# Kernel optimization log

Hardware: AMD Instinct MI355X
Metric: run time of the kernel (lower is better)

## Reference

```python
import jax, jax.numpy as jnp
import numpy as np

N_PEP = 50000
N_PROT = 50000
H = 256
F_IN = 1280
E = 300000
EL = 200000


def setup_inputs() -> dict:
    key = jax.random.key(0)
    ks = jax.random.split(key, 16)
    s = 0.02
    return {
        "x_pep": jax.random.normal(ks[0], (N_PEP, F_IN), jnp.float32),
        "x_prot": jax.random.normal(ks[1], (N_PROT, F_IN), jnp.float32),
        "Wpep": s * jax.random.normal(ks[2], (H, F_IN), jnp.float32),
        "bpep": jnp.zeros((H,), jnp.float32),
        "Wprot": s * jax.random.normal(ks[3], (H, F_IN), jnp.float32),
        "bprot": jnp.zeros((H,), jnp.float32),
        "Wl1": s * jax.random.normal(ks[4], (3, H, H), jnp.float32),
        "bl1": jnp.zeros((3, H), jnp.float32),
        "Wr1": s * jax.random.normal(ks[5], (3, H, H), jnp.float32),
        "Wl2": s * jax.random.normal(ks[6], (3, H, H), jnp.float32),
        "bl2": jnp.zeros((3, H), jnp.float32),
        "Wr2": s * jax.random.normal(ks[7], (3, H, H), jnp.float32),
        "ei_pp": jax.random.randint(ks[8], (2, E), 0, N_PEP, jnp.int32),   # pep -> prot
        "ei_rp": jax.random.randint(ks[9], (2, E), 0, N_PROT, jnp.int32),  # prot -> pep (reverse)
        "ei_prot": jax.random.randint(ks[10], (2, E), 0, N_PROT, jnp.int32),  # prot -> prot
        "eli_het": jax.random.randint(ks[11], (2, EL), 0, N_PEP, jnp.int32),
        "eli_homo": jax.random.randint(ks[12], (2, EL), 0, N_PROT, jnp.int32),
    }


def _seg_mean(src_feat, dst_idx, n_dst):
    # mean aggregation of edge messages into destination nodes
    s = jax.ops.segment_sum(src_feat, dst_idx, num_segments=n_dst)
    cnt = jax.ops.segment_sum(jnp.ones((dst_idx.shape[0], 1), src_feat.dtype), dst_idx, num_segments=n_dst)
    return s / jnp.maximum(cnt, 1.0)


def _sage(x_src, x_dst, ei, Wl, bl, Wr):
    # PyG SAGEConv(aggr='mean'): lin_l(mean_j x_j) + lin_r(x_i); lin_r has no bias
    m = _seg_mean(x_src[ei[0]], ei[1], x_dst.shape[0])
    return m @ Wl.T + bl + x_dst @ Wr.T


def reference(x_pep, x_prot, Wpep, bpep, Wprot, bprot,
              Wl1, bl1, Wr1, Wl2, bl2, Wr2,
              ei_pp, ei_rp, ei_prot, eli_het, eli_homo):
    # feat_src == 'esm': linear projection of ESM features
    h_pep = x_pep @ Wpep.T + bpep
    h_prot = x_prot @ Wprot.T + bprot

    # --- hetero SAGE layer 1 (to_hetero: sum over edge types per dst type) ---
    p1 = jax.nn.relu(_sage(h_prot, h_pep, ei_rp, Wl1[1], bl1[1], Wr1[1]))
    q1 = jax.nn.relu(_sage(h_pep, h_prot, ei_pp, Wl1[0], bl1[0], Wr1[0])
                     + _sage(h_prot, h_prot, ei_prot, Wl1[2], bl1[2], Wr1[2]))

    # --- hetero SAGE layer 2 ---
    p2 = _sage(q1, p1, ei_rp, Wl2[1], bl2[1], Wr2[1])
    q2 = (_sage(p1, q1, ei_pp, Wl2[0], bl2[0], Wr2[0])
          + _sage(q1, q1, ei_prot, Wl2[2], bl2[2], Wr2[2]))

    # edge classifiers: gather + elementwise mul + sum
    het_pred = (p2[eli_het[0]] * q2[eli_het[1]]).sum(axis=-1)
    homo_pred = (q2[eli_homo[0]] * q2[eli_homo[1]]).sum(axis=-1)
    return (het_pred, homo_pred)
```

## Files before the change

### kernel.cpp

```cpp
#include <hip/hip_runtime.h>

using u16 = unsigned short;
using u32 = unsigned int;

#define H 256
#define NNODE 50000
#define CAP 32
#define BM 128
#define BN 128
#define BK 64

typedef __attribute__((ext_vector_type(8))) short bf16x8;
typedef __attribute__((ext_vector_type(4))) float f32x4;

struct AChunks { const void* p[5]; };

__device__ __forceinline__ u16 f2b(float f) {
    u32 u = __builtin_bit_cast(u32, f);
    return (u16)((u + 0x7FFFu + ((u >> 16) & 1u)) >> 16);
}
__device__ __forceinline__ float b2f(u16 h) {
    u32 u = ((u32)h) << 16;
    return __builtin_bit_cast(float, u);
}
__device__ __forceinline__ void gld_lds16(const void* g, void* l) {
    __builtin_amdgcn_global_load_lds(
        (__attribute__((address_space(1))) void*)(void*)g,
        (__attribute__((address_space(3))) void*)l, 16, 0, 0);
}
__device__ __forceinline__ u32 packbf(float a, float b) {
    return (u32)f2b(a) | ((u32)f2b(b) << 16);
}

template<bool RELU>
__global__ __launch_bounds__(512) void gemm_pipe(
    AChunks ac, int aStride, const u16* __restrict__ Bw,
    const float* __restrict__ bias, u16* __restrict__ C, int M, int Ktot)
{
    __shared__ __align__(16) char As[2][BM * 128];
    __shared__ __align__(16) char Bs[2][BN * 128];

    const int tid = threadIdx.x;
    const int l   = tid & 63;
    const int w   = tid >> 6;
    const int wr  = w >> 2, wc = w & 3;
    const int m0  = blockIdx.x * BM;
    const int n0  = blockIdx.y * BN;
    const int nk  = Ktot >> 6;

    f32x4 acc[4][2];
#pragma unroll
    for (int i = 0; i < 4; ++i)
#pragma unroll
        for (int j = 0; j < 2; ++j) acc[i][j] = f32x4{0.f, 0.f, 0.f, 0.f};

    auto stageB = [&](int k, int bi) {
        int k0 = k * 64;
#pragma unroll
        for (int i = 0; i < 2; ++i) {
            int ci = i * 512 + tid;
            int r = ci >> 3, c16 = ci & 7;
            int sb = (c16 * 16) ^ ((r & 7) << 4);
            const u16* g = Bw + (size_t)(n0 + r) * Ktot + k0 + (sb >> 1);
            gld_lds16(g, &Bs[bi][ci * 16]);
        }
    };
    auto stageAb = [&](int k, int bi) {
        int k0 = k * 64;
        const u16* base = (const u16*)ac.p[k0 >> 8];
        int kk = k0 & 255;
#pragma unroll
        for (int i = 0; i < 2; ++i) {
            int ci = i * 512 + tid;
            int r = ci >> 3, c16 = ci & 7;
            int row = m0 + r; row = row < M ? row : M - 1;
            int sb = (c16 * 16) ^ ((r & 7) << 4);
            const u16* g = base + (size_t)row * aStride + kk + (sb >> 1);
            gld_lds16(g, &As[bi][ci * 16]);
        }
    };
    auto compute = [&](int bi) {
#pragma unroll
        for (int ks = 0; ks < 2; ++ks) {
            bf16x8 af[4], bfr[2];
#pragma unroll
            for (int mi = 0; mi < 4; ++mi) {
                int r = wr * 64 + mi * 16 + (l & 15);
                int off = (ks * 64 + (l >> 4) * 16) ^ ((r & 7) << 4);
                af[mi] = *(const bf16x8*)&As[bi][r * 128 + off];
            }
#pragma unroll
            for (int ni = 0; ni < 2; ++ni) {
                int r = wc * 32 + ni * 16 + (l & 15);
                int off = (ks * 64 + (l >> 4) * 16) ^ ((r & 7) << 4);
                bfr[ni] = *(const bf16x8*)&Bs[bi][r * 128 + off];
            }
#pragma unroll
            for (int mi = 0; mi < 4; ++mi)
#pragma unroll
                for (int ni = 0; ni < 2; ++ni)
                    acc[mi][ni] = __builtin_amdgcn_mfma_f32_16x16x32_bf16(
                        af[mi], bfr[ni], acc[mi][ni], 0, 0, 0);
        }
    };
    auto body = [&](int k, int cur) {
        asm volatile("s_waitcnt vmcnt(4)" ::: "memory");
        __builtin_amdgcn_sched_barrier(0);
        __builtin_amdgcn_s_barrier();
        __builtin_amdgcn_sched_barrier(0);
        compute(cur);
        __builtin_amdgcn_sched_barrier(0);
        __builtin_amdgcn_s_barrier();
        __builtin_amdgcn_sched_barrier(0);
        int kq = k + 2; if (kq > nk - 1) kq = nk - 1;
        stageB(kq, cur);
        stageAb(kq, cur);
        __builtin_amdgcn_sched_barrier(0);
    };

    stageB(0, 0); stageAb(0, 0);
    __builtin_amdgcn_sched_barrier(0);
    stageB(1, 1); stageAb(1, 1);
    __builtin_amdgcn_sched_barrier(0);
    for (int k = 0; k < nk; k += 2) {
        body(k,     0);
        body(k + 1, 1);
    }

    const int fr = l & 15, fq = l >> 4;
#pragma unroll
    for (int ni = 0; ni < 2; ++ni) {
        int col = n0 + wc * 32 + ni * 16 + fr;
        float bv = bias ? bias[col] : 0.f;
#pragma unroll
        for (int mi = 0; mi < 4; ++mi) {
            int rowb = m0 + wr * 64 + mi * 16 + fq * 4;
#pragma unroll
            for (int j = 0; j < 4; ++j) {
                int row = rowb + j;
                if (row < M) {
                    float v = acc[mi][ni][j] + bv;
                    if (RELU) v = fmaxf(v, 0.f);
                    C[(size_t)row * H + col] = f2b(v);
                }
            }
        }
    }
}

__global__ __launch_bounds__(256) void cvt_f32_bf16(
    const float* __restrict__ in, u16* __restrict__ outp, size_t n8)
{
    size_t i = (size_t)blockIdx.x * blockDim.x + threadIdx.x;
    size_t stride = (size_t)gridDim.x * blockDim.x;
    for (; i < n8; i += stride) {
        const float4* s = (const float4*)(in + i * 8);
        float4 v0 = s[0], v1 = s[1];
        uint4 o;
        o.x = packbf(v0.x, v0.y);
        o.y = packbf(v0.z, v0.w);
        o.z = packbf(v1.x, v1.y);
        o.w = packbf(v1.z, v1.w);
        *(uint4*)(outp + i * 8) = o;
    }
}

__global__ __launch_bounds__(256) void fill_zero(float4* __restrict__ p, size_t n4)
{
    size_t i = (size_t)blockIdx.x * blockDim.x + threadIdx.x;
    size_t stride = (size_t)gridDim.x * blockDim.x;
    for (; i < n4; i += stride) p[i] = make_float4(0.f, 0.f, 0.f, 0.f);
}

__global__ __launch_bounds__(256) void build_bucket(
    const int* __restrict__ src, const int* __restrict__ dst, int nE,
    int* __restrict__ cnt, int* __restrict__ bucket)
{
    int i = blockIdx.x * blockDim.x + threadIdx.x;
    if (i >= nE) return;
    int d = dst[i];
    int pos = atomicAdd(&cnt[d], 1);
    if (pos < CAP) bucket[(size_t)d * CAP + pos] = src[i];
}

__global__ __launch_bounds__(256) void seg_mean_gather(
    const u16* __restrict__ feat, const int* __restrict__ bucket,
    const int* __restrict__ cnt, int n_dst, u16* __restrict__ out)
{
    int d = (int)(((size_t)blockIdx.x * blockDim.x + threadIdx.x) >> 6);
    int lane = threadIdx.x & 63;
    if (d >= n_dst) return;
    int c = cnt[d];
    int cc = c < CAP ? c : CAP;
    const int* b = bucket + (size_t)d * CAP;
    float a0 = 0.f, a1 = 0.f, a2 = 0.f, a3 = 0.f;
    int i = 0;
    for (; i + 4 <= cc; i += 4) {
        int s0 = b[i], s1 = b[i + 1], s2 = b[i + 2], s3 = b[i + 3];
        uint2 v0 = *(const uint2*)(feat + (size_t)s0 * H + lane * 4);
        uint2 v1 = *(const uint2*)(feat + (size_t)s1 * H + lane * 4);
        uint2 v2 = *(const uint2*)(feat + (size_t)s2 * H + lane * 4);
        uint2 v3 = *(const uint2*)(feat + (size_t)s3 * H + lane * 4);
        a0 += b2f((u16)(v0.x & 0xffff)) + b2f((u16)(v1.x & 0xffff))
            + b2f((u16)(v2.x & 0xffff)) + b2f((u16)(v3.x & 0xffff));
        a1 += b2f((u16)(v0.x >> 16)) + b2f((u16)(v1.x >> 16))
            + b2f((u16)(v2.x >> 16)) + b2f((u16)(v3.x >> 16));
        a2 += b2f((u16)(v0.y & 0xffff)) + b2f((u16)(v1.y & 0xffff))
            + b2f((u16)(v2.y & 0xffff)) + b2f((u16)(v3.y & 0xffff));
        a3 += b2f((u16)(v0.y >> 16)) + b2f((u16)(v1.y >> 16))
            + b2f((u16)(v2.y >> 16)) + b2f((u16)(v3.y >> 16));
    }
    for (; i < cc; ++i) {
        uint2 v = *(const uint2*)(feat + (size_t)b[i] * H + lane * 4);
        a0 += b2f((u16)(v.x & 0xffff));
        a1 += b2f((u16)(v.x >> 16));
        a2 += b2f((u16)(v.y & 0xffff));
        a3 += b2f((u16)(v.y >> 16));
    }
    float inv = 1.0f / fmaxf((float)c, 1.0f);
    uint2 o;
    o.x = packbf(a0 * inv, a1 * inv);
    o.y = packbf(a2 * inv, a3 * inv);
    *(uint2*)(out + (size_t)d * H + lane * 4) = o;
}

__global__ __launch_bounds__(256) void edge_dot(
    const u16* __restrict__ P, const u16* __restrict__ Q,
    const int* __restrict__ ia, const int* __restrict__ ib,
    int nE, float* __restrict__ out)
{
    int gi = blockIdx.x * 256 + threadIdx.x;
    int e = gi >> 5, l32 = gi & 31;
    if (e >= nE) return;
    uint4 a = *(const uint4*)(P + (size_t)ia[e] * H + l32 * 8);
    uint4 b = *(const uint4*)(Q + (size_t)ib[e] * H + l32 * 8);
    float v = 0.f;
    v += b2f((u16)(a.x & 0xffff)) * b2f((u16)(b.x & 0xffff));
    v += b2f((u16)(a.x >> 16))    * b2f((u16)(b.x >> 16));
    v += b2f((u16)(a.y & 0xffff)) * b2f((u16)(b.y & 0xffff));
    v += b2f((u16)(a.y >> 16))    * b2f((u16)(b.y >> 16));
    v += b2f((u16)(a.z & 0xffff)) * b2f((u16)(b.z & 0xffff));
    v += b2f((u16)(a.z >> 16))    * b2f((u16)(b.z >> 16));
    v += b2f((u16)(a.w & 0xffff)) * b2f((u16)(b.w & 0xffff));
    v += b2f((u16)(a.w >> 16))    * b2f((u16)(b.w >> 16));
#pragma unroll
    for (int off = 16; off; off >>= 1) v += __shfl_xor(v, off);
    if (l32 == 0) out[e] = v;
}

struct PackTab {
    const float* s1[12]; const float* s2[12]; u16* dst[12];
    int Ks[12], Kdst[12], koff[12], blk0[13];
};
__global__ __launch_bounds__(256) void pack_all(PackTab t)
{
    int b = blockIdx.x;
    int it = 0;
    while (it < 11 && b >= t.blk0[it + 1]) ++it;
    int idx = (b - t.blk0[it]) * 1024 + threadIdx.x * 4;
    int Ks = t.Ks[it];
    if (idx >= 256 * Ks) return;
    int n = idx / Ks;
    int k = idx - n * Ks;
    float4 v = *(const float4*)(t.s1[it] + idx);
    if (t.s2[it]) {
        float4 u = *(const float4*)(t.s2[it] + idx);
        v.x += u.x; v.y += u.y; v.z += u.z; v.w += u.w;
    }
    ushort4 h;
    h.x = f2b(v.x); h.y = f2b(v.y); h.z = f2b(v.z); h.w = f2b(v.w);
    *(ushort4*)(t.dst[it] + (size_t)n * t.Kdst[it] + t.koff[it] + k) = h;
}

__global__ void bias_pair(const float* __restrict__ bl1, const float* __restrict__ bl2,
                          float* __restrict__ bq1, float* __restrict__ bq2)
{
    int i = threadIdx.x;
    if (blockIdx.x == 0) bq1[i] = bl1[i] + bl1[512 + i];
    else                 bq2[i] = bl2[i] + bl2[512 + i];
}

static inline void launch_gemm3(const void* a0, const void* a1, const void* a2,
                                const u16* Bw, const float* bias, u16* C,
                                int Ktot, bool relu, hipStream_t s)
{
    AChunks ac = {{a0, a1, a2, nullptr, nullptr}};
    dim3 grid((NNODE + BM - 1) / BM, H / BN);
    if (relu) gemm_pipe<true><<<grid, 512, 0, s>>>(ac, 256, Bw, bias, C, NNODE, Ktot);
    else      gemm_pipe<false><<<grid, 512, 0, s>>>(ac, 256, Bw, bias, C, NNODE, Ktot);
}

extern "C" void kernel_launch(void* const* d_in, const int* in_sizes, int n_in,
                              void* d_out, int out_size, void* d_ws, size_t ws_size,
                              hipStream_t stream)
{
    const float* x_pep  = (const float*)d_in[0];
    const float* x_prot = (const float*)d_in[1];
    const float* Wpep   = (const float*)d_in[2];
    const float* bpep   = (const float*)d_in[3];
    const float* Wprot  = (const float*)d_in[4];
    const float* bprot  = (const float*)d_in[5];
    const float* Wl1    = (const float*)d_in[6];
    const float* bl1    = (const float*)d_in[7];
    const float* Wr1    = (const float*)d_in[8];
    const float* Wl2    = (const float*)d_in[9];
    const float* bl2    = (const float*)d_in[10];
    const float* Wr2    = (const float*)d_in[11];
    const int* ei_pp    = (const int*)d_in[12];
    const int* ei_rp    = (const int*)d_in[13];
    const int* ei_prot  = (const int*)d_in[14];
    const int* eli_het  = (const int*)d_in[15];
    const int* eli_homo = (const int*)d_in[16];

    const int E  = in_sizes[12] / 2;
    const int EL = in_sizes[15] / 2;
    const int FIN = in_sizes[2] / H;

    float* out = (float*)d_out;

    const size_t nodeElems = (size_t)NNODE * H;
    u16* bufA = (u16*)d_ws;
    u16* bufB = bufA + nodeElems;
    u16* bufC = bufB + nodeElems;
    u16* bufD = bufC + nodeElems;
    u16* bufE = bufD + nodeElems;
    u16* bufF = bufE + nodeElems;
    u16* Bpep  = bufF + nodeElems;
    u16* Bprot = Bpep  + (size_t)256 * 1280;
    u16* Bp1   = Bprot + (size_t)256 * 1280;
    u16* Bq1   = Bp1   + (size_t)256 * 512;
    u16* Bp2   = Bq1   + (size_t)256 * 768;
    u16* Bq2   = Bp2   + (size_t)256 * 512;
    float* bq1 = (float*)(Bq2 + (size_t)256 * 768);
    float* bq2 = bq1 + 256;
    int* cntRP   = (int*)(bq2 + 256);
    int* cntPP   = cntRP + NNODE;
    int* cntPR   = cntPP + NNODE;
    int* bktRP   = cntPR + NNODE;
    int* bktPP   = bktRP + (size_t)NNODE * CAP;
    int* bktPR   = bktPP + (size_t)NNODE * CAP;
    u16* xbPep   = (u16*)(bktPR + (size_t)NNODE * CAP);
    u16* xbProt  = xbPep + (size_t)NNODE * 1280;

    const size_t HH = (size_t)H * H;

    PackTab t{};
    int blk = 0, it = 0;
    auto add = [&](const float* s1, const float* s2, u16* d, int Ks, int Kd, int ko) {
        t.s1[it] = s1; t.s2[it] = s2; t.dst[it] = d;
        t.Ks[it] = Ks; t.Kdst[it] = Kd; t.koff[it] = ko;
        t.blk0[it] = blk; blk += (256 * Ks) / 1024; ++it;
    };
    add(Wpep,  nullptr, Bpep,  1280, 1280, 0);
    add(Wprot, nullptr, Bprot, 1280, 1280, 0);
    add(Wl1 + 1 * HH, nullptr,      Bp1, 256, 512, 0);
    add(Wr1 + 1 * HH, nullptr,      Bp1, 256, 512, 256);
    add(Wl1 + 0 * HH, nullptr,      Bq1, 256, 768, 0);
    add(Wl1 + 2 * HH, nullptr,      Bq1, 256, 768, 256);
    add(Wr1 + 0 * HH, Wr1 + 2 * HH, Bq1, 256, 768, 512);
    add(Wl2 + 1 * HH, nullptr,      Bp2, 256, 512, 0);
    add(Wr2 + 1 * HH, nullptr,      Bp2, 256, 512, 256);
    add(Wl2 + 0 * HH, nullptr,      Bq2, 256, 768, 0);
    add(Wl2 + 2 * HH, nullptr,      Bq2, 256, 768, 256);
    add(Wr2 + 0 * HH, Wr2 + 2 * HH, Bq2, 256, 768, 512);
    t.blk0[12] = blk;
    pack_all<<<blk, 256, 0, stream>>>(t);
    bias_pair<<<2, 256, 0, stream>>>(bl1, bl2, bq1, bq2);

    fill_zero<<<147, 256, 0, stream>>>((float4*)cntRP, (size_t)3 * NNODE / 4);
    build_bucket<<<(E + 255) / 256, 256, 0, stream>>>(ei_rp,   ei_rp + E,   E, cntRP, bktRP);
    build_bucket<<<(E + 255) / 256, 256, 0, stream>>>(ei_pp,   ei_pp + E,   E, cntPP, bktPP);
    build_bucket<<<(E + 255) / 256, 256, 0, stream>>>(ei_prot, ei_prot + E, E, cntPR, bktPR);

    {
        const size_t n8 = (size_t)NNODE * FIN / 8;
        cvt_f32_bf16<<<2048, 256, 0, stream>>>(x_pep,  xbPep,  n8);
        cvt_f32_bf16<<<2048, 256, 0, stream>>>(x_prot, xbProt, n8);
        dim3 grid((NNODE + BM - 1) / BM, H / BN);
        AChunks ap = {{xbPep, xbPep + 256, xbPep + 512, xbPep + 768, xbPep + 1024}};
        gemm_pipe<false><<<grid, 512, 0, stream>>>(ap, FIN, Bpep, bpep, bufA, NNODE, FIN);
        AChunks aq = {{xbProt, xbProt + 256, xbProt + 512, xbProt + 768, xbProt + 1024}};
        gemm_pipe<false><<<grid, 512, 0, stream>>>(aq, FIN, Bprot, bprot, bufB, NNODE, FIN);
    }

    const int gG = (NNODE * 64 + 255) / 256;
    seg_mean_gather<<<gG, 256, 0, stream>>>(bufB, bktRP, cntRP, NNODE, bufE);
    launch_gemm3(bufE, bufA, nullptr, Bp1, bl1 + 256, bufC, 512, true, stream);
    seg_mean_gather<<<gG, 256, 0, stream>>>(bufA, bktPP, cntPP, NNODE, bufE);
    seg_mean_gather<<<gG, 256, 0, stream>>>(bufB, bktPR, cntPR, NNODE, bufF);
    launch_gemm3(bufE, bufF, bufB, Bq1, bq1, bufD, 768, true, stream);

    seg_mean_gather<<<gG, 256, 0, stream>>>(bufD, bktRP, cntRP, NNODE, bufE);
    launch_gemm3(bufE, bufC, nullptr, Bp2, bl2 + 256, bufA, 512, false, stream);
    seg_mean_gather<<<gG, 256, 0, stream>>>(bufC, bktPP, cntPP, NNODE, bufE);
    seg_mean_gather<<<gG, 256, 0, stream>>>(bufD, bktPR, cntPR, NNODE, bufF);
    launch_gemm3(bufE, bufF, bufD, Bq2, bq2, bufB, 768, false, stream);

    edge_dot<<<(EL * 32 + 255) / 256, 256, 0, stream>>>(bufA, bufB, eli_het,  eli_het  + EL, EL, out);
    edge_dot<<<(EL * 32 + 255) / 256, 256, 0, stream>>>(bufB, bufB, eli_homo, eli_homo + EL, EL, out + EL);
}
```

Before: 752.4 us.

## Convert input features into K-tiled bf16 layout for contiguous GEMM A loads

```diff
diff --git a/kernel.cpp b/kernel.cpp
--- a/kernel.cpp
+++ b/kernel.cpp
@@ -9,11 +9,13 @@
 #define BM 128
 #define BN 128
 #define BK 64
+#define FINK 1280
+#define NB 1563
 
 typedef __attribute__((ext_vector_type(8))) short bf16x8;
 typedef __attribute__((ext_vector_type(4))) float f32x4;
 
-struct AChunks { const void* p[5]; };
+struct AChunks { const void* p[3]; };
 
 __device__ __forceinline__ u16 f2b(float f) {
     u32 u = __builtin_bit_cast(u32, f);
@@ -32,7 +34,7 @@
     return (u32)f2b(a) | ((u32)f2b(b) << 16);
 }
 
-template<bool RELU>
+template<bool TILED, bool RELU>
 __global__ __launch_bounds__(512) void gemm_pipe(
     AChunks ac, int aStride, const u16* __restrict__ Bw,
     const float* __restrict__ bias, u16* __restrict__ C, int M, int Ktot)
@@ -65,18 +67,32 @@
             gld_lds16(g, &Bs[bi][ci * 16]);
         }
     };
-    auto stageAb = [&](int k, int bi) {
-        int k0 = k * 64;
-        const u16* base = (const u16*)ac.p[k0 >> 8];
-        int kk = k0 & 255;
-#pragma unroll
-        for (int i = 0; i < 2; ++i) {
-            int ci = i * 512 + tid;
-            int r = ci >> 3, c16 = ci & 7;
-            int row = m0 + r; row = row < M ? row : M - 1;
-            int sb = (c16 * 16) ^ ((r & 7) << 4);
-            const u16* g = base + (size_t)row * aStride + kk + (sb >> 1);
-            gld_lds16(g, &As[bi][ci * 16]);
+    auto stageA = [&](int k, int bi) {
+        if (!TILED) {
+            int k0 = k * 64;
+            const u16* base = (const u16*)ac.p[k0 >> 8];
+            int kk = k0 & 255;
+#pragma unroll
+            for (int i = 0; i < 2; ++i) {
+                int ci = i * 512 + tid;
+                int r = ci >> 3, c16 = ci & 7;
+                int row = m0 + r; row = row < M ? row : M - 1;
+                int sb = (c16 * 16) ^ ((r & 7) << 4);
+                const u16* g = base + (size_t)row * aStride + kk + (sb >> 1);
+                gld_lds16(g, &As[bi][ci * 16]);
+            }
+        } else {
+            const u16* base = (const u16*)ac.p[0];
+#pragma unroll
+            for (int i = 0; i < 2; ++i) {
+                int ci = i * 512 + tid;
+                int r = ci >> 3, c16 = ci & 7;
+                int R = m0 + r; R = R < M ? R : M - 1;
+                int sb = (c16 * 16) ^ ((R & 7) << 4);
+                const u16* g = base + ((size_t)k * NB + (R >> 5)) * 2048
+                                    + (R & 31) * 64 + (sb >> 1);
+                gld_lds16(g, &As[bi][ci * 16]);
+            }
         }
     };
     auto compute = [&](int bi) {
@@ -114,13 +130,13 @@
         __builtin_amdgcn_sched_barrier(0);
         int kq = k + 2; if (kq > nk - 1) kq = nk - 1;
         stageB(kq, cur);
-        stageAb(kq, cur);
+        stageA(kq, cur);
         __builtin_amdgcn_sched_barrier(0);
     };
 
-    stageB(0, 0); stageAb(0, 0);
+    stageB(0, 0); stageA(0, 0);
     __builtin_amdgcn_sched_barrier(0);
-    stageB(1, 1); stageAb(1, 1);
+    stageB(1, 1); stageA(1, 1);
     __builtin_amdgcn_sched_barrier(0);
     for (int k = 0; k < nk; k += 2) {
         body(k,     0);
@@ -148,20 +164,33 @@
     }
 }
 
-__global__ __launch_bounds__(256) void cvt_f32_bf16(
-    const float* __restrict__ in, u16* __restrict__ outp, size_t n8)
-{
-    size_t i = (size_t)blockIdx.x * blockDim.x + threadIdx.x;
-    size_t stride = (size_t)gridDim.x * blockDim.x;
-    for (; i < n8; i += stride) {
-        const float4* s = (const float4*)(in + i * 8);
-        float4 v0 = s[0], v1 = s[1];
-        uint4 o;
-        o.x = packbf(v0.x, v0.y);
-        o.y = packbf(v0.z, v0.w);
-        o.z = packbf(v1.x, v1.y);
-        o.w = packbf(v1.z, v1.w);
-        *(uint4*)(outp + i * 8) = o;
+__global__ __launch_bounds__(256) void cvt_tile(
+    const float* __restrict__ in, u16* __restrict__ outp, int M)
+{
+    __shared__ __align__(16) char lds[32 * 2560];
+    const int b = blockIdx.x;
+    const int r0 = b * 32;
+    const int tid = threadIdx.x;
+
+    const float* src = in + (size_t)r0 * FINK;
+    const int lastRows = M - r0;
+    for (int c = tid; c < (32 * FINK) / 4; c += 256) {
+        int elem = c * 4;
+        int row = elem / FINK;
+        float4 v = make_float4(0.f, 0.f, 0.f, 0.f);
+        if (row < lastRows) v = *(const float4*)(src + elem);
+        uint2 pr;
+        pr.x = packbf(v.x, v.y);
+        pr.y = packbf(v.z, v.w);
+        *(uint2*)(lds + (size_t)elem * 2) = pr;
+    }
+    __syncthreads();
+
+    const int row = tid >> 3, k16 = tid & 7;
+    for (int t = 0; t < FINK / 64; ++t) {
+        uint4 v = *(const uint4*)(lds + row * 2560 + t * 128 + k16 * 16);
+        u16* dst = outp + ((size_t)t * NB + b) * 2048 + row * 64 + k16 * 8;
+        *(uint4*)dst = v;
     }
 }
 
@@ -284,10 +313,10 @@
                                 const u16* Bw, const float* bias, u16* C,
                                 int Ktot, bool relu, hipStream_t s)
 {
-    AChunks ac = {{a0, a1, a2, nullptr, nullptr}};
+    AChunks ac = {{a0, a1, a2}};
     dim3 grid((NNODE + BM - 1) / BM, H / BN);
-    if (relu) gemm_pipe<true><<<grid, 512, 0, s>>>(ac, 256, Bw, bias, C, NNODE, Ktot);
-    else      gemm_pipe<false><<<grid, 512, 0, s>>>(ac, 256, Bw, bias, C, NNODE, Ktot);
+    if (relu) gemm_pipe<false, true><<<grid, 512, 0, s>>>(ac, 256, Bw, bias, C, NNODE, Ktot);
+    else      gemm_pipe<false, false><<<grid, 512, 0, s>>>(ac, 256, Bw, bias, C, NNODE, Ktot);
 }
 
 extern "C" void kernel_launch(void* const* d_in, const int* in_sizes, int n_in,
@@ -314,7 +343,6 @@
 
     const int E  = in_sizes[12] / 2;
     const int EL = in_sizes[15] / 2;
-    const int FIN = in_sizes[2] / H;
 
     float* out = (float*)d_out;
 
@@ -340,7 +368,7 @@
     int* bktPP   = bktRP + (size_t)NNODE * CAP;
     int* bktPR   = bktPP + (size_t)NNODE * CAP;
     u16* xbPep   = (u16*)(bktPR + (size_t)NNODE * CAP);
-    u16* xbProt  = xbPep + (size_t)NNODE * 1280;
+    u16* xbProt  = xbPep + (size_t)20 * NB * 2048;
 
     const size_t HH = (size_t)H * H;
 
@@ -373,14 +401,13 @@
     build_bucket<<<(E + 255) / 256, 256, 0, stream>>>(ei_prot, ei_prot + E, E, cntPR, bktPR);
 
     {
-        const size_t n8 = (size_t)NNODE * FIN / 8;
-        cvt_f32_bf16<<<2048, 256, 0, stream>>>(x_pep,  xbPep,  n8);
-        cvt_f32_bf16<<<2048, 256, 0, stream>>>(x_prot, xbProt, n8);
         dim3 grid((NNODE + BM - 1) / BM, H / BN);
-        AChunks ap = {{xbPep, xbPep + 256, xbPep + 512, xbPep + 768, xbPep + 1024}};
-        gemm_pipe<false><<<grid, 512, 0, stream>>>(ap, FIN, Bpep, bpep, bufA, NNODE, FIN);
-        AChunks aq = {{xbProt, xbProt + 256, xbProt + 512, xbProt + 768, xbProt + 1024}};
-        gemm_pipe<false><<<grid, 512, 0, stream>>>(aq, FIN, Bprot, bprot, bufB, NNODE, FIN);
+        AChunks ap = {{xbPep, nullptr, nullptr}};
+        AChunks aq = {{xbProt, nullptr, nullptr}};
+        cvt_tile<<<NB, 256, 0, stream>>>(x_pep,  xbPep,  NNODE);
+        gemm_pipe<true, false><<<grid, 512, 0, stream>>>(ap, 0, Bpep, bpep, bufA, NNODE, FINK);
+        cvt_tile<<<NB, 256, 0, stream>>>(x_prot, xbProt, NNODE);
+        gemm_pipe<true, false><<<grid, 512, 0, stream>>>(aq, 0, Bprot, bprot, bufB, NNODE, FINK);
     }
 
     const int gG = (NNODE * 64 + 255) / 256;
```

Result: slower. 809.7 us (+7.6%).

## Widen GEMM tile to full N=256 with K32 steps and chunk input projection

Applied to the files above, without the earlier changes.

```diff
diff --git a/kernel.cpp b/kernel.cpp
--- a/kernel.cpp
+++ b/kernel.cpp
@@ -6,9 +6,11 @@
 #define H 256
 #define NNODE 50000
 #define CAP 32
-#define BM 128
-#define BN 128
-#define BK 64
+#define FINK 1280
+#define CHUNK 25088
+
+#define ASEG 2080
+#define BSEG 4128
 
 typedef __attribute__((ext_vector_type(8))) short bf16x8;
 typedef __attribute__((ext_vector_type(4))) float f32x4;
@@ -33,78 +35,67 @@
 }
 
 template<bool RELU>
-__global__ __launch_bounds__(512) void gemm_pipe(
+__global__ __launch_bounds__(512) void gemm_k32(
     AChunks ac, int aStride, const u16* __restrict__ Bw,
     const float* __restrict__ bias, u16* __restrict__ C, int M, int Ktot)
 {
-    __shared__ __align__(16) char As[2][BM * 128];
-    __shared__ __align__(16) char Bs[2][BN * 128];
+    __shared__ __align__(16) char As[2][4 * ASEG];
+    __shared__ __align__(16) char Bs[2][4 * BSEG];
 
     const int tid = threadIdx.x;
     const int l   = tid & 63;
     const int w   = tid >> 6;
     const int wr  = w >> 2, wc = w & 3;
-    const int m0  = blockIdx.x * BM;
-    const int n0  = blockIdx.y * BN;
-    const int nk  = Ktot >> 6;
-
-    f32x4 acc[4][2];
+    const int m0  = blockIdx.x * 128;
+    const int nk  = Ktot >> 5;
+
+    f32x4 acc[4][4];
 #pragma unroll
     for (int i = 0; i < 4; ++i)
 #pragma unroll
-        for (int j = 0; j < 2; ++j) acc[i][j] = f32x4{0.f, 0.f, 0.f, 0.f};
-
+        for (int j = 0; j < 4; ++j) acc[i][j] = f32x4{0.f, 0.f, 0.f, 0.f};
+
+    auto stageA = [&](int k, int bi) {
+        int k0 = k * 32;
+        const u16* base = (const u16*)ac.p[k0 >> 8];
+        int kk = k0 & 255;
+        int ks = tid >> 7, r = tid & 127;
+        int row = m0 + r; row = row < M ? row : M - 1;
+        const u16* g = base + (size_t)row * aStride + kk + ks * 8;
+        gld_lds16(g, &As[bi][ks * ASEG + r * 16]);
+    };
     auto stageB = [&](int k, int bi) {
-        int k0 = k * 64;
+        int k0 = k * 32;
 #pragma unroll
         for (int i = 0; i < 2; ++i) {
             int ci = i * 512 + tid;
-            int r = ci >> 3, c16 = ci & 7;
-            int sb = (c16 * 16) ^ ((r & 7) << 4);
-            const u16* g = Bw + (size_t)(n0 + r) * Ktot + k0 + (sb >> 1);
-            gld_lds16(g, &Bs[bi][ci * 16]);
+            int ks = ci >> 8, r = ci & 255;
+            const u16* g = Bw + (size_t)r * Ktot + k0 + ks * 8;
+            gld_lds16(g, &Bs[bi][ks * BSEG + r * 16]);
         }
     };
-    auto stageAb = [&](int k, int bi) {
-        int k0 = k * 64;
-        const u16* base = (const u16*)ac.p[k0 >> 8];
-        int kk = k0 & 255;
-#pragma unroll
-        for (int i = 0; i < 2; ++i) {
-            int ci = i * 512 + tid;
-            int r = ci >> 3, c16 = ci & 7;
-            int row = m0 + r; row = row < M ? row : M - 1;
-            int sb = (c16 * 16) ^ ((r & 7) << 4);
-            const u16* g = base + (size_t)row * aStride + kk + (sb >> 1);
-            gld_lds16(g, &As[bi][ci * 16]);
+    auto compute = [&](int bi) {
+        const int ksl = l >> 4;
+        bf16x8 af[4], bfr[4];
+#pragma unroll
+        for (int mi = 0; mi < 4; ++mi) {
+            int r = wr * 64 + mi * 16 + (l & 15);
+            af[mi] = *(const bf16x8*)&As[bi][ksl * ASEG + r * 16];
         }
-    };
-    auto compute = [&](int bi) {
-#pragma unroll
-        for (int ks = 0; ks < 2; ++ks) {
-            bf16x8 af[4], bfr[2];
-#pragma unroll
-            for (int mi = 0; mi < 4; ++mi) {
-                int r = wr * 64 + mi * 16 + (l & 15);
-                int off = (ks * 64 + (l >> 4) * 16) ^ ((r & 7) << 4);
-                af[mi] = *(const bf16x8*)&As[bi][r * 128 + off];
-            }
-#pragma unroll
-            for (int ni = 0; ni < 2; ++ni) {
-                int r = wc * 32 + ni * 16 + (l & 15);
-                int off = (ks * 64 + (l >> 4) * 16) ^ ((r & 7) << 4);
-                bfr[ni] = *(const bf16x8*)&Bs[bi][r * 128 + off];
-            }
-#pragma unroll
-            for (int mi = 0; mi < 4; ++mi)
-#pragma unroll
-                for (int ni = 0; ni < 2; ++ni)
-                    acc[mi][ni] = __builtin_amdgcn_mfma_f32_16x16x32_bf16(
-                        af[mi], bfr[ni], acc[mi][ni], 0, 0, 0);
+#pragma unroll
+        for (int ni = 0; ni < 4; ++ni) {
+            int r = wc * 64 + ni * 16 + (l & 15);
+            bfr[ni] = *(const bf16x8*)&Bs[bi][ksl * BSEG + r * 16];
         }
+#pragma unroll
+        for (int mi = 0; mi < 4; ++mi)
+#pragma unroll
+            for (int ni = 0; ni < 4; ++ni)
+                acc[mi][ni] = __builtin_amdgcn_mfma_f32_16x16x32_bf16(
+                    af[mi], bfr[ni], acc[mi][ni], 0, 0, 0);
     };
     auto body = [&](int k, int cur) {
-        asm volatile("s_waitcnt vmcnt(4)" ::: "memory");
+        asm volatile("s_waitcnt vmcnt(3)" ::: "memory");
         __builtin_amdgcn_sched_barrier(0);
         __builtin_amdgcn_s_barrier();
         __builtin_amdgcn_sched_barrier(0);
@@ -114,24 +105,25 @@
         __builtin_amdgcn_sched_barrier(0);
         int kq = k + 2; if (kq > nk - 1) kq = nk - 1;
         stageB(kq, cur);
-        stageAb(kq, cur);
-        __builtin_amdgcn_sched_barrier(0);
-    };
-
-    stageB(0, 0); stageAb(0, 0);
+        stageA(kq, cur);
+        __builtin_amdgcn_sched_barrier(0);
+    };
+
+    stageB(0, 0); stageA(0, 0);
     __builtin_amdgcn_sched_barrier(0);
-    stageB(1, 1); stageAb(1, 1);
+    stageB(1, 1); stageA(1, 1);
     __builtin_amdgcn_sched_barrier(0);
     for (int k = 0; k < nk; k += 2) {
         body(k,     0);
         body(k + 1, 1);
     }
+    asm volatile("s_waitcnt vmcnt(0)" ::: "memory");
 
     const int fr = l & 15, fq = l >> 4;
 #pragma unroll
-    for (int ni = 0; ni < 2; ++ni) {
-        int col = n0 + wc * 32 + ni * 16 + fr;
-        float bv = bias ? bias[col] : 0.f;
+    for (int ni = 0; ni < 4; ++ni) {
+        int col = wc * 64 + ni * 16 + fr;
+        float bv = bias[col];
 #pragma unroll
         for (int mi = 0; mi < 4; ++mi) {
             int rowb = m0 + wr * 64 + mi * 16 + fq * 4;
@@ -285,9 +277,9 @@
                                 int Ktot, bool relu, hipStream_t s)
 {
     AChunks ac = {{a0, a1, a2, nullptr, nullptr}};
-    dim3 grid((NNODE + BM - 1) / BM, H / BN);
-    if (relu) gemm_pipe<true><<<grid, 512, 0, s>>>(ac, 256, Bw, bias, C, NNODE, Ktot);
-    else      gemm_pipe<false><<<grid, 512, 0, s>>>(ac, 256, Bw, bias, C, NNODE, Ktot);
+    dim3 grid((NNODE + 127) / 128, 1);
+    if (relu) gemm_k32<true><<<grid, 512, 0, s>>>(ac, 256, Bw, bias, C, NNODE, Ktot);
+    else      gemm_k32<false><<<grid, 512, 0, s>>>(ac, 256, Bw, bias, C, NNODE, Ktot);
 }
 
 extern "C" void kernel_launch(void* const* d_in, const int* in_sizes, int n_in,
@@ -314,7 +306,6 @@
 
     const int E  = in_sizes[12] / 2;
     const int EL = in_sizes[15] / 2;
-    const int FIN = in_sizes[2] / H;
 
     float* out = (float*)d_out;
 
@@ -339,8 +330,7 @@
     int* bktRP   = cntPR + NNODE;
     int* bktPP   = bktRP + (size_t)NNODE * CAP;
     int* bktPR   = bktPP + (size_t)NNODE * CAP;
-    u16* xbPep   = (u16*)(bktPR + (size_t)NNODE * CAP);
-    u16* xbProt  = xbPep + (size_t)NNODE * 1280;
+    u16* xb      = (u16*)(bktPR + (size_t)NNODE * CAP);
 
     const size_t HH = (size_t)H * H;
 
@@ -373,14 +363,20 @@
     build_bucket<<<(E + 255) / 256, 256, 0, stream>>>(ei_prot, ei_prot + E, E, cntPR, bktPR);
 
     {
-        const size_t n8 = (size_t)NNODE * FIN / 8;
-        cvt_f32_bf16<<<2048, 256, 0, stream>>>(x_pep,  xbPep,  n8);
-        cvt_f32_bf16<<<2048, 256, 0, stream>>>(x_prot, xbProt, n8);
-        dim3 grid((NNODE + BM - 1) / BM, H / BN);
-        AChunks ap = {{xbPep, xbPep + 256, xbPep + 512, xbPep + 768, xbPep + 1024}};
-        gemm_pipe<false><<<grid, 512, 0, stream>>>(ap, FIN, Bpep, bpep, bufA, NNODE, FIN);
-        AChunks aq = {{xbProt, xbProt + 256, xbProt + 512, xbProt + 768, xbProt + 1024}};
-        gemm_pipe<false><<<grid, 512, 0, stream>>>(aq, FIN, Bprot, bprot, bufB, NNODE, FIN);
+        auto proj = [&](const float* x, const u16* Bw, const float* bias, u16* Cout) {
+            int offs[3] = {0, CHUNK, NNODE};
+            for (int c = 0; c < 2; ++c) {
+                int r0 = offs[c], rows = offs[c + 1] - r0;
+                cvt_f32_bf16<<<2048, 256, 0, stream>>>(
+                    x + (size_t)r0 * FINK, xb, (size_t)rows * FINK / 8);
+                AChunks ac = {{xb, xb + 256, xb + 512, xb + 768, xb + 1024}};
+                dim3 grid((rows + 127) / 128, 1);
+                gemm_k32<false><<<grid, 512, 0, stream>>>(
+                    ac, FINK, Bw, bias, Cout + (size_t)r0 * H, rows, FINK);
+            }
+        };
+        proj(x_pep,  Bpep,  bpep,  bufA);
+        proj(x_prot, Bprot, bprot, bufB);
     }
 
     const int gG = (NNODE * 64 + 255) / 256;
```

New measurement: 909.2 us. 20.8% more time.
